# Optimization experiments

Measured on AMD Instinct MI355X. Metric: run time of the kernel, lower is better.

Reference implementation:

```python
import jax, jax.numpy as jnp
import numpy as np

B, T, V, E, D, F = 128, 64, 10000, 512, 512, 2048


def setup_inputs() -> dict:
    key = jax.random.key(0)
    ks = iter(jax.random.split(key, 40))
    def nrm(shape, s=0.02):
        return (jax.random.normal(next(ks), shape, jnp.float32) * s)
    inp = {
        "image_vectors": jax.random.normal(next(ks), (B, F), jnp.float32),
        "captions_ix": jax.random.randint(next(ks), (B, T), 0, V),
        "emb": nrm((V, E)),
        "W_init_h1": nrm((D, F)), "b_init_h1": jnp.zeros((D,), jnp.float32),
        "W_init_c1": nrm((D, F)), "b_init_c1": jnp.zeros((D,), jnp.float32),
        "W_init_h2": nrm((D, F)), "b_init_h2": jnp.zeros((D,), jnp.float32),
        "W_init_c2": nrm((D, F)), "b_init_c2": jnp.zeros((D,), jnp.float32),
        "W_ih1": nrm((4 * D, E)), "W_hh1": nrm((4 * D, D)), "b1": jnp.zeros((4 * D,), jnp.float32),
        "W_ih2": nrm((4 * D, 2 * D)), "W_hh2": nrm((4 * D, D)), "b2": jnp.zeros((4 * D,), jnp.float32),
        "Wv1": nrm((D, D)), "bv1": jnp.zeros((D,), jnp.float32),
        "Wo1": nrm((D, D)), "bo1": jnp.zeros((D,), jnp.float32),
        "Wv2": nrm((D, D)), "bv2": jnp.zeros((D,), jnp.float32),
        "Wo2": nrm((D, D)), "bo2": jnp.zeros((D,), jnp.float32),
        "W_logits": nrm((V, 3 * D)), "b_logits": jnp.zeros((V,), jnp.float32),
    }
    return inp


def _lstm(x, h0, c0, W_ih, W_hh, b):
    # x: [B,T,Din] -> hidden states [B,T,D]; PyTorch gate order (i,f,g,o), b = b_ih + b_hh.
    xp = jnp.einsum('btd,gd->btg', x, W_ih) + b  # precompute input projections
    def step(carry, xt):
        h, c = carry
        gates = xt + h @ W_hh.T
        i, f, g, o = jnp.split(gates, 4, axis=-1)
        c = jax.nn.sigmoid(f) * c + jax.nn.sigmoid(i) * jnp.tanh(g)
        h = jax.nn.sigmoid(o) * jnp.tanh(c)
        return (h, c), h
    _, hs = jax.lax.scan(step, (h0, c0), jnp.swapaxes(xp, 0, 1))
    return jnp.swapaxes(hs, 0, 1)


def reference(image_vectors, captions_ix, emb,
              W_init_h1, b_init_h1, W_init_c1, b_init_c1,
              W_init_h2, b_init_h2, W_init_c2, b_init_c2,
              W_ih1, W_hh1, b1, W_ih2, W_hh2, b2,
              Wv1, bv1, Wo1, bo1, Wv2, bv2, Wo2, bo2,
              W_logits, b_logits):
    h1 = image_vectors @ W_init_h1.T + b_init_h1
    c1 = image_vectors @ W_init_c1.T + b_init_c1
    h2 = image_vectors @ W_init_h2.T + b_init_h2
    c2 = image_vectors @ W_init_c2.T + b_init_c2
    x = emb[captions_ix]  # [B,T,E] (dropout p=0 -> identity)
    h1s = _lstm(x, h1, c1, W_ih1, W_hh1, b1)  # [B,T,D]; LSTM output == hidden state
    # MHA with key=value of length 1: softmax over one key is exactly 1, so the
    # output is out_proj(v_proj(key)) independent of the (growing prefix) query.
    attn1 = (h1s @ Wv1.T + bv1) @ Wo1.T + bo1  # [B,T,D]
    h2s = _lstm(jnp.concatenate([h1s, attn1], axis=-1), h2, c2, W_ih2, W_hh2, b2)
    attn2 = (h2s @ Wv2.T + bv2) @ Wo2.T + bo2
    out = jnp.concatenate([h2s, attn1, attn2], axis=-1)  # [B,T,3D]
    return out @ W_logits.T + b_logits  # [B,T,V]
```

## Files before the change

### kernel.cpp

```cpp
#include <hip/hip_runtime.h>
#include <stdint.h>

#define DEV __device__ __forceinline__

typedef short bf16x8 __attribute__((ext_vector_type(8)));
typedef float f32x4 __attribute__((ext_vector_type(4)));

DEV unsigned short f2bf(float f) {
  union { float f; uint32_t u; } v; v.f = f;
  return (unsigned short)((v.u + 0x7fffu + ((v.u >> 16) & 1u)) >> 16);
}
DEV float bf2f(unsigned short u) {
  union { uint32_t u; float f; } v; v.u = (uint32_t)u << 16; return v.f;
}

DEV float fsig(float x) { return 1.f / (1.f + __expf(-x)); }
DEV float ftanh(float x) { float e = __expf(2.f * x); return 1.f - 2.f / (e + 1.f); }

DEV void gload16(const void* g, void* lds) {
  __builtin_amdgcn_global_load_lds(
      (const __attribute__((address_space(1))) int*)(uintptr_t)g,
      (__attribute__((address_space(3))) int*)(uintptr_t)lds, 16, 0, 0);
}

template <int MODE>
__global__ __launch_bounds__(256) void gemm_nt(
    const unsigned short* __restrict__ A, int lda,
    const unsigned short* __restrict__ B, int ldb,
    void* __restrict__ P0, void* __restrict__ P1,
    void* __restrict__ P2, void* __restrict__ P3,
    int ldc, int ldc2,
    const float* __restrict__ bias,
    int K, int Nreal)
{
  __shared__ alignas(16) unsigned short Asm[128 * 32];
  __shared__ alignas(16) unsigned short Bsm[128 * 32];
  const int tid = threadIdx.x;
  const int wave = tid >> 6, lane = tid & 63;

  const int gx = gridDim.x;
  const int lin = blockIdx.y * gx + blockIdx.x;
  const int nwg = gx * gridDim.y;
  const int q = nwg >> 3, r = nwg & 7;
  const int xcd = lin & 7, i2 = lin >> 3;
  const int wg = (xcd < r ? xcd * (q + 1) : r * (q + 1) + (xcd - r) * q) + i2;
  const int m0 = (wg % gx) * 128, n0 = (wg / gx) * 128;

  const int wr = wave >> 1, wc = wave & 1;
  f32x4 acc[4][4] = {};

  const int q0 = tid, q1 = tid + 256;
  const unsigned short* Ag0 = A + (size_t)(m0 + (q0 >> 2)) * lda + (q0 & 3) * 8;
  const unsigned short* Ag1 = A + (size_t)(m0 + (q1 >> 2)) * lda + (q1 & 3) * 8;
  const unsigned short* Bg0 = B + (size_t)(n0 + (q0 >> 2)) * ldb + (q0 & 3) * 8;
  const unsigned short* Bg1 = B + (size_t)(n0 + (q1 >> 2)) * ldb + (q1 & 3) * 8;
  char* As0 = (char*)Asm + wave * 1024;  char* As1 = As0 + 4096;
  char* Bs0 = (char*)Bsm + wave * 1024;  char* Bs1 = Bs0 + 4096;

  const int ra = wr * 64 + (lane & 15);
  const int rb = wc * 64 + (lane & 15);
  const int kb = (lane >> 4) * 16;

  for (int k0 = 0; k0 < K; k0 += 32) {
    gload16(Ag0 + k0, As0);
    gload16(Ag1 + k0, As1);
    gload16(Bg0 + k0, Bs0);
    gload16(Bg1 + k0, Bs1);
    __syncthreads();
    bf16x8 af[4], bfr[4];
#pragma unroll
    for (int i = 0; i < 4; ++i)
      af[i] = *(const bf16x8*)((const char*)Asm + (ra + i * 16) * 64 + kb);
#pragma unroll
    for (int i = 0; i < 4; ++i)
      bfr[i] = *(const bf16x8*)((const char*)Bsm + (rb + i * 16) * 64 + kb);
#pragma unroll
    for (int mi = 0; mi < 4; ++mi)
#pragma unroll
      for (int ni = 0; ni < 4; ++ni)
        acc[mi][ni] = __builtin_amdgcn_mfma_f32_16x16x32_bf16(af[mi], bfr[ni], acc[mi][ni], 0, 0, 0);
    __syncthreads();
  }

  const int row0 = m0 + wr * 64 + (lane >> 4) * 4;
  const int col0 = n0 + wc * 64 + (lane & 15);

  if constexpr (MODE == 2) {
#pragma unroll
    for (int mi = 0; mi < 4; ++mi) {
      const int rowb = row0 + mi * 16;
      const int dd = rowb >> 2;
      const float4 b4 = *(const float4*)&bias[rowb];
#pragma unroll
      for (int ni = 0; ni < 4; ++ni) {
        const int col = col0 + ni * 16;
        const int tt = col & 63, bb = col >> 6;
        float4 v;
        v.x = acc[mi][ni][0] + b4.x;
        v.y = acc[mi][ni][1] + b4.y;
        v.z = acc[mi][ni][2] + b4.z;
        v.w = acc[mi][ni][3] + b4.w;
        const int wgid = (bb >> 4) * 16 + (dd >> 5);
        const int ww = (dd >> 3) & 3, mi2 = (dd >> 2) & 1, ln = (dd & 3) * 16 + (bb & 15);
        ((float4*)P0)[((((size_t)tt * 128 + wgid) * 4 + ww) * 2 + mi2) * 64 + ln] = v;
      }
    }
    return;
  }

#pragma unroll
  for (int mi = 0; mi < 4; ++mi) {
#pragma unroll
    for (int ni = 0; ni < 4; ++ni) {
      const int col = col0 + ni * 16;
      if (col >= Nreal) continue;
      const float bs = bias ? bias[col] : 0.f;
#pragma unroll
      for (int rr = 0; rr < 4; ++rr) {
        const int row = row0 + mi * 16 + rr;
        const float v = acc[mi][ni][rr] + bs;
        if constexpr (MODE == 1) {
          ((unsigned short*)P0)[(size_t)row * ldc + col] = f2bf(v);
          if (P1) ((unsigned short*)P1)[(size_t)row * ldc2 + col] = f2bf(v);
        } else if constexpr (MODE == 4) {
          const unsigned short ad = ((const unsigned short*)P1)[(size_t)row * ldc2 + col];
          ((unsigned short*)P0)[(size_t)row * ldc + col] = f2bf(v + bf2f(ad));
        } else {
          const int seg = col >> 9, cc = col & 511;
          if (seg == 0)      ((unsigned short*)P0)[(size_t)row * 512 + cc] = f2bf(v);
          else if (seg == 1) ((float*)P1)[(size_t)row * 512 + cc] = v;
          else if (seg == 2) ((unsigned short*)P2)[(size_t)row * 512 + cc] = f2bf(v);
          else               ((float*)P3)[(size_t)row * 512 + cc] = v;
        }
      }
    }
  }
}

__global__ __launch_bounds__(512, 2) void gemm256(
    const unsigned short* __restrict__ A, int lda,
    const unsigned short* __restrict__ B, int ldb,
    float* __restrict__ C, int ldc,
    const float* __restrict__ bias, int K, int Nreal)
{
  __shared__ alignas(16) unsigned short Lds[2][2][16384];
  const int tid = threadIdx.x;
  const int wave = tid >> 6, lane = tid & 63;
  const int fr = lane & 15, kq = lane >> 4;

  const int gx = gridDim.x;
  const int lin = blockIdx.y * gx + blockIdx.x;
  const int nwg = gx * gridDim.y;
  const int q8 = nwg >> 3, r8 = nwg & 7;
  const int xcd = lin & 7, i2 = lin >> 3;
  const int wg = (xcd < r8 ? xcd * (q8 + 1) : r8 * (q8 + 1) + (xcd - r8) * q8) + i2;
  const int m0 = (wg % gx) * 256, n0 = (wg / gx) * 256;

  const int wr = wave >> 2, wc = wave & 3;

  const unsigned short* srcA[4];
  const unsigned short* srcB[4];
  int dstO[4];
#pragma unroll
  for (int s = 0; s < 4; ++s) {
    const int c = tid + s * 512;
    const int row = c >> 3, qp = (c & 7) ^ (row & 7);
    srcA[s] = A + (size_t)(m0 + row) * lda + qp * 8;
    srcB[s] = B + (size_t)(n0 + row) * ldb + qp * 8;
    dstO[s] = (wave * 64 + s * 512) * 16;
  }

  const int NT = K >> 6;
#define STAGE256(kt, buf)                                            \
  {                                                                  \
    _Pragma("unroll")                                                \
    for (int s = 0; s < 4; ++s)                                      \
      gload16(srcA[s] + (kt) * 64, (char*)&Lds[buf][0][0] + dstO[s]);\
    _Pragma("unroll")                                                \
    for (int s = 0; s < 4; ++s)                                      \
      gload16(srcB[s] + (kt) * 64, (char*)&Lds[buf][1][0] + dstO[s]);\
  }
  STAGE256(0, 0);
  STAGE256(1, 1);

  f32x4 acc[8][4] = {};
  const int slot0 = (kq ^ (fr & 7)) * 16;

  for (int kt = 0; kt < NT; ++kt) {
    asm volatile("s_waitcnt vmcnt(8)" ::: "memory");
    __builtin_amdgcn_sched_barrier(0);
    __builtin_amdgcn_s_barrier();
    __builtin_amdgcn_sched_barrier(0);
    const char* bufA = (const char*)&Lds[kt & 1][0][0];
    const char* bufB = (const char*)&Lds[kt & 1][1][0];
    bf16x8 Bf[4][2];
#pragma unroll
    for (int n = 0; n < 4; ++n) {
      const char* bb = bufB + (wc * 64 + n * 16 + fr) * 128;
      Bf[n][0] = *(const bf16x8*)(bb + slot0);
      Bf[n][1] = *(const bf16x8*)(bb + (slot0 ^ 64));
    }
#pragma unroll
    for (int q = 0; q < 4; ++q) {
      bf16x8 Af[2][2];
#pragma unroll
      for (int m2 = 0; m2 < 2; ++m2) {
        const char* ab = bufA + (wr * 128 + q * 32 + m2 * 16 + fr) * 128;
        Af[m2][0] = *(const bf16x8*)(ab + slot0);
        Af[m2][1] = *(const bf16x8*)(ab + (slot0 ^ 64));
      }
      __builtin_amdgcn_s_setprio(1);
#pragma unroll
      for (int m2 = 0; m2 < 2; ++m2)
#pragma unroll
        for (int n = 0; n < 4; ++n) {
          acc[q * 2 + m2][n] = __builtin_amdgcn_mfma_f32_16x16x32_bf16(
              Af[m2][0], Bf[n][0], acc[q * 2 + m2][n], 0, 0, 0);
          acc[q * 2 + m2][n] = __builtin_amdgcn_mfma_f32_16x16x32_bf16(
              Af[m2][1], Bf[n][1], acc[q * 2 + m2][n], 0, 0, 0);
        }
      __builtin_amdgcn_s_setprio(0);
    }
    __builtin_amdgcn_sched_barrier(0);
    __builtin_amdgcn_s_barrier();
    __builtin_amdgcn_sched_barrier(0);
    const int kn = (kt + 2 < NT) ? kt + 2 : 0;
    STAGE256(kn, kt & 1);
  }

#pragma unroll
  for (int mf = 0; mf < 8; ++mf) {
    const int row = m0 + wr * 128 + mf * 16 + kq * 4;
#pragma unroll
    for (int n = 0; n < 4; ++n) {
      const int col = n0 + wc * 64 + n * 16 + fr;
      if (col < Nreal) {
        const float bs = bias[col];
#pragma unroll
        for (int rr = 0; rr < 4; ++rr)
          __builtin_nontemporal_store(acc[mf][n][rr] + bs,
                                      &C[(size_t)(row + rr) * ldc + col]);
      }
    }
  }
#undef STAGE256
}

__global__ __launch_bounds__(256, 1) void lstm_fused(
    const unsigned short* __restrict__ Whh1, const unsigned short* __restrict__ Whh2,
    const unsigned short* __restrict__ Weff2r,
    const unsigned short* __restrict__ h01, const unsigned short* __restrict__ h02,
    const float* __restrict__ c1st, const float* __restrict__ c2st,
    const float* __restrict__ xpr,
    const float* __restrict__ beff2,
    unsigned short* __restrict__ hx1, unsigned short* __restrict__ hx2,
    unsigned short* __restrict__ hcat,
    int* __restrict__ flags)
{
  __shared__ unsigned short Wsm[8][128][64];
  __shared__ uint32_t Hst[16][16];
  const int tid = threadIdx.x;
  const bool role2 = blockIdx.x >= 128;
  const int wg = role2 ? blockIdx.x - 128 : blockIdx.x;
  const int g = wg >> 4, s = wg & 15;
  const int w = tid >> 6, lane = tid & 63, fr = lane & 15, kq = lane >> 4;

  {
    const unsigned short* Whh = role2 ? Whh2 : Whh1;
    const int m = tid >> 1;
    const int row = (m & 3) * 512 + s * 32 + (m >> 2);
    const unsigned short* src = Whh + (size_t)row * 512 + (tid & 1) * 256;
#pragma unroll 4
    for (int cc = 0; cc < 32; ++cc) {
      const int k = (tid & 1) * 256 + cc * 8;
      uint4 v = *(const uint4*)(src + cc * 8);
      const int kblk = k >> 6, c = (k & 63) >> 3, sl = c ^ (m & 7);
      *(uint4*)((char*)&Wsm[kblk][m][0] + sl * 16) = v;
    }
  }

  const int b = g * 16 + fr;
  const int d0 = s * 32 + w * 8 + kq;
  const float* c0 = role2 ? c2st : c1st;
  float c_r[2];
  c_r[0] = c0[b * 512 + d0];
  c_r[1] = c0[b * 512 + d0 + 4];
  __syncthreads();

  int* fl1 = flags + g * 16;
  int* fl2 = flags + 128 + g * 16;
  int* flown = role2 ? fl2 : fl1;
  unsigned short* hxown = role2 ? hx2 : hx1;
  const unsigned short* hinit = role2 ? h02 : h01;
  const int colbase = (role2 ? 0 : 512) + s * 32;
  const float4* xv = (const float4*)xpr + ((size_t)(wg * 4 + w) * 2) * 64 + lane;
  float4 be0 = {0, 0, 0, 0}, be1 = {0, 0, 0, 0};
  if (role2) {
    be0 = *(const float4*)(beff2 + s * 128 + w * 32 + kq * 4);
    be1 = *(const float4*)(beff2 + s * 128 + w * 32 + 16 + kq * 4);
  }
  const size_t hxg = (size_t)g * 8192;

  for (int t = 0; t < 64; ++t) {
    f32x4 acc[2] = {};
    float4 xg0, xg1;

    if (!role2) {
      xg0 = xv[(size_t)t * 65536];
      xg1 = xv[(size_t)t * 65536 + 64];
      if (t) {
        if (w == 1) {
          for (;;) {
            bool ok = true;
            if (lane < 16)
              ok = __hip_atomic_load(fl1 + lane, __ATOMIC_RELAXED,
                                     __HIP_MEMORY_SCOPE_AGENT) >= t;
            if (__all(ok)) break;
            __builtin_amdgcn_s_sleep(1);
          }
        }
        __syncthreads();
      }
      bf16x8 hf[16];
      if (t == 0) {
#pragma unroll
        for (int kk = 0; kk < 16; ++kk)
          hf[kk] = *(const bf16x8*)(hinit + (size_t)b * 512 + kk * 32 + kq * 8);
      } else {
        const unsigned short* hb = hx1 + (size_t)(t - 1) * 65536 + hxg + fr * 32 + kq * 8;
#pragma unroll
        for (int kk = 0; kk < 16; ++kk)
          hf[kk] = *(const bf16x8*)(hb + kk * 512);
      }
#pragma unroll
      for (int kk = 0; kk < 16; ++kk) {
        const int kblk = kk >> 1, cbase = (kk & 1) * 4 + kq;
#pragma unroll
        for (int mi = 0; mi < 2; ++mi) {
          const int m = w * 32 + mi * 16 + fr;
          const int sl = cbase ^ (m & 7);
          const bf16x8 af = *(const bf16x8*)((const char*)&Wsm[kblk][m][0] + sl * 16);
          acc[mi] = __builtin_amdgcn_mfma_f32_16x16x32_bf16(af, hf[kk], acc[mi], 0, 0, 0);
        }
      }
    } else {
      xg0 = be0; xg1 = be1;
      if (w == 1) {
        for (;;) {
          bool ok = true;
          if (lane < 16)
            ok = __hip_atomic_load(fl1 + lane, __ATOMIC_RELAXED,
                                   __HIP_MEMORY_SCOPE_AGENT) >= t + 1;
          if (__all(ok)) break;
          __builtin_amdgcn_s_sleep(1);
        }
      }
      __syncthreads();
      const unsigned short* h1b = hx1 + (size_t)t * 65536 + hxg + fr * 32 + kq * 8;
      bf16x8 hf1[16];
#pragma unroll
      for (int kk = 0; kk < 16; ++kk)
        hf1[kk] = *(const bf16x8*)(h1b + kk * 512);
      const bf16x8* wr = (const bf16x8*)Weff2r + (size_t)s * 32 * 256 + tid;
#pragma unroll
      for (int kk = 0; kk < 8; ++kk) {
#pragma unroll
        for (int mi = 0; mi < 2; ++mi)
          acc[mi] = __builtin_amdgcn_mfma_f32_16x16x32_bf16(
              wr[(kk * 2 + mi) * 256], hf1[kk], acc[mi], 0, 0, 0);
      }
      if (t) {
        if (w == 1) {
          for (;;) {
            bool ok = true;
            if (lane < 16)
              ok = __hip_atomic_load(fl2 + lane, __ATOMIC_RELAXED,
                                     __HIP_MEMORY_SCOPE_AGENT) >= t;
            if (__all(ok)) break;
            __builtin_amdgcn_s_sleep(1);
          }
        }
        __syncthreads();
      }
      bf16x8 hf2[16];
      if (t == 0) {
#pragma unroll
        for (int kk = 0; kk < 16; ++kk)
          hf2[kk] = *(const bf16x8*)(hinit + (size_t)b * 512 + kk * 32 + kq * 8);
      } else {
        const unsigned short* hb = hx2 + (size_t)(t - 1) * 65536 + hxg + fr * 32 + kq * 8;
#pragma unroll
        for (int kk = 0; kk < 16; ++kk)
          hf2[kk] = *(const bf16x8*)(hb + kk * 512);
      }
#pragma unroll
      for (int kk = 8; kk < 16; ++kk) {
#pragma unroll
        for (int mi = 0; mi < 2; ++mi)
          acc[mi] = __builtin_amdgcn_mfma_f32_16x16x32_bf16(
              wr[(kk * 2 + mi) * 256], hf1[kk], acc[mi], 0, 0, 0);
      }
#pragma unroll
      for (int kk = 0; kk < 16; ++kk) {
        const int kblk = kk >> 1, cbase = (kk & 1) * 4 + kq;
#pragma unroll
        for (int mi = 0; mi < 2; ++mi) {
          const int m = w * 32 + mi * 16 + fr;
          const int sl = cbase ^ (m & 7);
          const bf16x8 af = *(const bf16x8*)((const char*)&Wsm[kblk][m][0] + sl * 16);
          acc[mi] = __builtin_amdgcn_mfma_f32_16x16x32_bf16(af, hf2[kk], acc[mi], 0, 0, 0);
        }
      }
    }

    unsigned short hn[2];
#pragma unroll
    for (int mi = 0; mi < 2; ++mi) {
      const float4 xg = mi ? xg1 : xg0;
      const float iv = acc[mi][0] + xg.x;
      const float fv = acc[mi][1] + xg.y;
      const float gv = acc[mi][2] + xg.z;
      const float ov = acc[mi][3] + xg.w;
      const float c = fsig(fv) * c_r[mi] + fsig(iv) * ftanh(gv);
      c_r[mi] = c;
      hn[mi] = f2bf(fsig(ov) * ftanh(c));
    }

    const uint32_t pk = (uint32_t)hn[0] | ((uint32_t)hn[1] << 16);
    const uint32_t y = (uint32_t)__shfl_xor((int)pk, 16);
    const uint32_t word = (kq & 1) ? __builtin_amdgcn_perm(pk, y, 0x07060302)
                                   : __builtin_amdgcn_perm(y, pk, 0x05040100);
    Hst[fr][w * 4 + ((kq & 1) ? 2 + (kq >> 1) : (kq >> 1))] = word;
    __syncthreads();

    if (w == 0) {
      const uint4 v = *(const uint4*)&Hst[lane >> 2][(lane & 3) * 4];
      unsigned short* dst = hxown + (size_t)t * 65536 + hxg + s * 512 + lane * 8;
      __hip_atomic_store((unsigned long long*)dst, ((const unsigned long long*)&v)[0],
                         __ATOMIC_RELAXED, __HIP_MEMORY_SCOPE_AGENT);
      __hip_atomic_store((unsigned long long*)(dst + 4), ((const unsigned long long*)&v)[1],
                         __ATOMIC_RELAXED, __HIP_MEMORY_SCOPE_AGENT);
      asm volatile("s_waitcnt vmcnt(0)" ::: "memory");
      if (lane == 0)
        __hip_atomic_store(flown + s, t + 1, __ATOMIC_RELAXED, __HIP_MEMORY_SCOPE_AGENT);
      const int row = (g * 16 + (lane >> 2)) * 64 + t;
      *(uint4*)(hcat + (size_t)row * 1024 + colbase + (lane & 3) * 8) = v;
    }
  }
}

struct CastJobs {
  const float* src[12];
  unsigned short* dst[12];
  long nreal4[12];
  long cum4[13];
  int n;
};

__global__ void cast_multi4(CastJobs J) {
  const long total = J.cum4[J.n];
  for (long i = (long)blockIdx.x * blockDim.x + threadIdx.x; i < total;
       i += (long)gridDim.x * blockDim.x) {
    int s = 0;
    while (i >= J.cum4[s + 1]) ++s;
    const long off = i - J.cum4[s];
    float4 v = {0.f, 0.f, 0.f, 0.f};
    if (off < J.nreal4[s]) v = ((const float4*)J.src[s])[off];
    ushort4 o;
    o.x = f2bf(v.x); o.y = f2bf(v.y); o.z = f2bf(v.z); o.w = f2bf(v.w);
    ((ushort4*)J.dst[s])[off] = o;
  }
}

__global__ void prep1(const float* __restrict__ Wv1, const float* __restrict__ Wv2,
                      const float* __restrict__ Wihl1, const float* __restrict__ Wihl2,
                      const float* __restrict__ b1, const float* __restrict__ b2,
                      const float* __restrict__ bih1, const float* __restrict__ bic1,
                      const float* __restrict__ bih2, const float* __restrict__ bic2,
                      const float* __restrict__ Wo1, const float* __restrict__ bv1,
                      const float* __restrict__ bo1,
                      const float* __restrict__ Wo2, const float* __restrict__ bv2,
                      const float* __restrict__ bo2,
                      unsigned short* __restrict__ WvT1, unsigned short* __restrict__ WvT2,
                      unsigned short* __restrict__ Wp1, unsigned short* __restrict__ Wp2,
                      float* __restrict__ bp1, float* __restrict__ bp2,
                      float* __restrict__ bcat,
                      float* __restrict__ bc1, float* __restrict__ bc2)
{
  const long NTOT = 924672;
  for (long id = (long)blockIdx.x * blockDim.x + threadIdx.x; id < NTOT;
       id += (long)gridDim.x * blockDim.x) {
    if (id < 131072) {
      const int m = (int)(id >> 6), kb = (int)(id & 63) * 8;
      const float* sp = Wihl1 + (size_t)((m & 3) * 512 + (m >> 2)) * 512 + kb;
      unsigned short o[8];
#pragma unroll
      for (int e = 0; e < 8; ++e) o[e] = f2bf(sp[e]);
      *(uint4*)(Wp1 + (size_t)m * 512 + kb) = *(const uint4*)o;
    } else if (id < 393216) {
      const long j = id - 131072;
      const int m = (int)(j >> 7), kb = (int)(j & 127) * 8;
      const float* sp = Wihl2 + (size_t)((m & 3) * 512 + (m >> 2)) * 1024 + kb;
      unsigned short o[8];
#pragma unroll
      for (int e = 0; e < 8; ++e) o[e] = f2bf(sp[e]);
      *(uint4*)(Wp2 + (size_t)m * 1024 + kb) = *(const uint4*)o;
    } else if (id < 917504) {
      const long t = id - 393216;
      const int which = (int)(t >> 18);
      const int u = (int)(t & 262143), a = u >> 9, bb = u & 511;
      (which ? WvT2 : WvT1)[u] = f2bf((which ? Wv2 : Wv1)[(size_t)bb * 512 + a]);
    } else if (id < 921600) {
      const int t = (int)(id - 917504);
      if (t < 2048) bp1[t] = b1[(t & 3) * 512 + (t >> 2)];
      else { const int m = t - 2048; bp2[m] = b2[(m & 3) * 512 + (m >> 2)]; }
    } else if (id < 923648) {
      const int i = (int)(id - 921600);
      const float* sarr[4] = {bih1, bic1, bih2, bic2};
      bcat[i] = sarr[i >> 9][i & 511];
    } else {
      const int i = (int)(id - 923648);
      const float* Wo = (i >= 512) ? Wo2 : Wo1;
      const float* bv = (i >= 512) ? bv2 : bv1;
      const float* bo = (i >= 512) ? bo2 : bo1;
      float* bc = (i >= 512) ? bc2 : bc1;
      const int r = i & 511;
      float sacc = bo[r];
      for (int k = 0; k < 512; k += 4) {
        const float4 wv = *(const float4*)(Wo + (size_t)r * 512 + k);
        const float4 bb = *(const float4*)(bv + k);
        sacc += wv.x * bb.x + wv.y * bb.y + wv.z * bb.z + wv.w * bb.w;
      }
      bc[r] = sacc;
    }
  }
}

__global__ void gather_rows(const int* __restrict__ ix, const float* __restrict__ emb,
                            unsigned short* __restrict__ x) {
  const int row = blockIdx.x;
  const int e = ix[row];
  const float4* s = (const float4*)(emb + (size_t)e * 512) + threadIdx.x * 2;
  const float4 a = s[0], b = s[1];
  unsigned short o[8] = {f2bf(a.x), f2bf(a.y), f2bf(a.z), f2bf(a.w),
                         f2bf(b.x), f2bf(b.y), f2bf(b.z), f2bf(b.w)};
  *(uint4*)(x + (size_t)row * 512 + threadIdx.x * 8) = *(const uint4*)o;
}

__global__ void reorder_wbf(const unsigned short* __restrict__ W,
                            unsigned short* __restrict__ R) {
  const int id = blockIdx.x * blockDim.x + threadIdx.x;
  const int tid = id & 255, mi = (id >> 8) & 1, kk = (id >> 9) & 15, s = id >> 13;
  const int w = tid >> 6, lane = tid & 63, fr = lane & 15, kq = lane >> 4;
  const int row = s * 128 + w * 32 + mi * 16 + fr;
  const int col = kk * 32 + kq * 8;
  *((uint4*)R + id) = *(const uint4*)(W + (size_t)row * 512 + col);
}

__global__ void bias2(const unsigned short* __restrict__ Wl, const float* __restrict__ blog,
                      const unsigned short* __restrict__ Wp2, const float* __restrict__ bp2,
                      const float* __restrict__ bc1, const float* __restrict__ bc2,
                      float* __restrict__ blcat, float* __restrict__ beff2) {
  const int lane = threadIdx.x & 63;
  if (blockIdx.x < 512) {
    const int m = blockIdx.x * 4 + (threadIdx.x >> 6);
    const unsigned short* row = Wp2 + (size_t)m * 1024 + 512;
    float sum = 0.f;
    for (int k = lane; k < 512; k += 64) sum += bf2f(row[k]) * bc1[k];
#pragma unroll
    for (int mm = 32; mm; mm >>= 1) sum += __shfl_xor(sum, mm, 64);
    if (lane == 0) beff2[m] = bp2[m] + sum;
  } else {
    const int j = (blockIdx.x - 512) * 4 + (threadIdx.x >> 6);
    const unsigned short* row = Wl + (size_t)j * 1536;
    float sum = 0.f;
    for (int k = lane; k < 512; k += 64) {
      sum += bf2f(row[512 + k]) * bc1[k];
      sum += bf2f(row[1024 + k]) * bc2[k];
    }
#pragma unroll
    for (int mm = 32; mm; mm >>= 1) sum += __shfl_xor(sum, mm, 64);
    if (lane == 0) blcat[j] = blog[j] + sum;
  }
}

extern "C" void kernel_launch(void* const* d_in, const int* in_sizes, int n_in,
                              void* d_out, int out_size, void* d_ws, size_t ws_size,
                              hipStream_t stream) {
  (void)in_sizes; (void)n_in; (void)out_size; (void)ws_size;
  const float* img    = (const float*)d_in[0];
  const int*   ix     = (const int*)d_in[1];
  const float* emb    = (const float*)d_in[2];
  const float* Wih1f  = (const float*)d_in[3];
  const float* bih1   = (const float*)d_in[4];
  const float* Wic1f  = (const float*)d_in[5];
  const float* bic1   = (const float*)d_in[6];
  const float* Wih2f  = (const float*)d_in[7];
  const float* bih2   = (const float*)d_in[8];
  const float* Wic2f  = (const float*)d_in[9];
  const float* bic2   = (const float*)d_in[10];
  const float* Wihl1  = (const float*)d_in[11];
  const float* Whhl1  = (const float*)d_in[12];
  const float* b1     = (const float*)d_in[13];
  const float* Wihl2  = (const float*)d_in[14];
  const float* Whhl2  = (const float*)d_in[15];
  const float* b2     = (const float*)d_in[16];
  const float* Wv1    = (const float*)d_in[17];
  const float* bv1    = (const float*)d_in[18];
  const float* Wo1    = (const float*)d_in[19];
  const float* bo1    = (const float*)d_in[20];
  const float* Wv2    = (const float*)d_in[21];
  const float* bv2    = (const float*)d_in[22];
  const float* Wo2    = (const float*)d_in[23];
  const float* bo2    = (const float*)d_in[24];
  const float* Wlog   = (const float*)d_in[25];
  const float* blog   = (const float*)d_in[26];
  float* out = (float*)d_out;

  char* p = (char*)d_ws;
  auto al = [&](size_t bytes) { char* r = p; p += (bytes + 255) & ~(size_t)255; return r; };
  unsigned short* Wp1    = (unsigned short*)al((size_t)2048 * 512 * 2);
  unsigned short* Whh1_b = (unsigned short*)al((size_t)2048 * 512 * 2);
  unsigned short* Wp2    = (unsigned short*)al((size_t)2048 * 1024 * 2);
  unsigned short* Whh2_b = (unsigned short*)al((size_t)2048 * 512 * 2);
  unsigned short* WvT1   = (unsigned short*)al((size_t)512 * 512 * 2);
  unsigned short* Wo1_b  = (unsigned short*)al((size_t)512 * 512 * 2);
  unsigned short* WvT2   = (unsigned short*)al((size_t)512 * 512 * 2);
  unsigned short* Wo2_b  = (unsigned short*)al((size_t)512 * 512 * 2);
  unsigned short* Wc1T   = (unsigned short*)al((size_t)512 * 512 * 2);
  unsigned short* Wc2T   = (unsigned short*)al((size_t)512 * 512 * 2);
  unsigned short* Wlog_b = (unsigned short*)al((size_t)10240 * 1536 * 2);
  unsigned short* Wcat   = (unsigned short*)al((size_t)10240 * 1024 * 2);
  unsigned short* Weff2  = (unsigned short*)al((size_t)2048 * 512 * 2);
  unsigned short* Weff2r = (unsigned short*)al((size_t)2048 * 512 * 2);
  unsigned short* Wh1i_b = (unsigned short*)al((size_t)512 * 2048 * 2);
  unsigned short* Wc1i_b = (unsigned short*)al((size_t)512 * 2048 * 2);
  unsigned short* Wh2i_b = (unsigned short*)al((size_t)512 * 2048 * 2);
  unsigned short* Wc2i_b = (unsigned short*)al((size_t)512 * 2048 * 2);
  unsigned short* img_b  = (unsigned short*)al((size_t)128 * 2048 * 2);
  unsigned short* x_b    = (unsigned short*)al((size_t)8192 * 512 * 2);
  float*          xpr    = (float*)al((size_t)8192 * 2048 * 4);
  unsigned short* hcat   = (unsigned short*)al((size_t)8192 * 1024 * 2);
  unsigned short* hx1    = (unsigned short*)al((size_t)64 * 128 * 512 * 2);
  unsigned short* hx2    = (unsigned short*)al((size_t)64 * 128 * 512 * 2);
  unsigned short* h01    = (unsigned short*)al((size_t)128 * 512 * 2);
  unsigned short* h02    = (unsigned short*)al((size_t)128 * 512 * 2);
  float*          c1st   = (float*)al((size_t)128 * 512 * 4);
  float*          c2st   = (float*)al((size_t)128 * 512 * 4);
  float*          bcat   = (float*)al((size_t)2048 * 4);
  float*          bp1    = (float*)al((size_t)2048 * 4);
  float*          bp2    = (float*)al((size_t)2048 * 4);
  float*          bc1    = (float*)al((size_t)512 * 4);
  float*          bc2    = (float*)al((size_t)512 * 4);
  float*          beff2  = (float*)al((size_t)2048 * 4);
  float*          blcat  = (float*)al((size_t)10240 * 4);
  int*            flags  = (int*)al(2048);

  hipMemsetAsync(flags, 0, 2048, stream);

  CastJobs J = {};
  auto addjob = [&](const float* s, unsigned short* d, long nreal, long ntot) {
    J.src[J.n] = s; J.dst[J.n] = d; J.nreal4[J.n] = nreal / 4;
    J.cum4[J.n + 1] = J.cum4[J.n] + ntot / 4; ++J.n;
  };
  addjob(img,   img_b,  (long)128 * 2048,   (long)128 * 2048);
  addjob(Whhl1, Whh1_b, (long)2048 * 512,   (long)2048 * 512);
  addjob(Whhl2, Whh2_b, (long)2048 * 512,   (long)2048 * 512);
  addjob(Wo1,   Wo1_b,  (long)512 * 512,    (long)512 * 512);
  addjob(Wo2,   Wo2_b,  (long)512 * 512,    (long)512 * 512);
  addjob(Wih1f, Wh1i_b, (long)512 * 2048,   (long)512 * 2048);
  addjob(Wic1f, Wc1i_b, (long)512 * 2048,   (long)512 * 2048);
  addjob(Wih2f, Wh2i_b, (long)512 * 2048,   (long)512 * 2048);
  addjob(Wic2f, Wc2i_b, (long)512 * 2048,   (long)512 * 2048);
  addjob(Wlog,  Wlog_b, (long)10000 * 1536, (long)10240 * 1536);
  cast_multi4<<<2048, 256, 0, stream>>>(J);

  prep1<<<1024, 256, 0, stream>>>(Wv1, Wv2, Wihl1, Wihl2, b1, b2,
                                  bih1, bic1, bih2, bic2,
                                  Wo1, bv1, bo1, Wo2, bv2, bo2,
                                  WvT1, WvT2, Wp1, Wp2, bp1, bp2, bcat, bc1, bc2);

  gather_rows<<<8192, 64, 0, stream>>>(ix, emb, x_b);

  gemm_nt<1><<<dim3(4, 4), 256, 0, stream>>>(
      WvT1, 512, Wo1_b, 512, Wc1T, nullptr, nullptr, nullptr, 512, 0, nullptr, 512, 512);
  gemm_nt<1><<<dim3(4, 4), 256, 0, stream>>>(
      WvT2, 512, Wo2_b, 512, Wc2T, nullptr, nullptr, nullptr, 512, 0, nullptr, 512, 512);

  gemm_nt<4><<<dim3(16, 4), 256, 0, stream>>>(
      Wp2 + 512, 1024, Wc1T, 512, Weff2, Wp2, nullptr, nullptr, 512, 1024, nullptr, 512, 512);
  reorder_wbf<<<512, 256, 0, stream>>>(Weff2, Weff2r);
  bias2<<<3012, 256, 0, stream>>>(Wlog_b, blog, Wp2, bp2, bc1, bc2, blcat, beff2);

  gemm_nt<4><<<dim3(80, 4), 256, 0, stream>>>(
      Wlog_b + 1024, 1536, Wc2T, 512, Wcat, Wlog_b, nullptr, nullptr, 1024, 1536,
      nullptr, 512, 512);
  gemm_nt<1><<<dim3(80, 4), 256, 0, stream>>>(
      Wlog_b + 512, 1536, Wc1T, 512, Wcat + 512, nullptr, nullptr, nullptr, 1024, 0,
      nullptr, 512, 512);

  gemm_nt<3><<<dim3(1, 16), 256, 0, stream>>>(
      img_b, 2048, Wh1i_b, 2048, h01, c1st, h02, c2st, 0, 0, bcat, 2048, 2048);

  gemm_nt<2><<<dim3(16, 64), 256, 0, stream>>>(
      Wp1, 512, x_b, 512, xpr, nullptr, nullptr, nullptr, 0, 0, bp1, 512, 8192);

  lstm_fused<<<256, 256, 0, stream>>>(
      Whh1_b, Whh2_b, Weff2r, h01, h02, c1st, c2st, xpr, beff2, hx1, hx2, hcat, flags);

  gemm256<<<dim3(32, 40), 512, 0, stream>>>(
      hcat, 1024, Wcat, 1024, out, 10000, blcat, 1024, 10000);
}
```

Measured before the change: 842.6 us.

## Batch independent prep GEMMs into grouped launches and merge small prep kernels

Replaces the templated per-mode gemm_nt launches with a gemm_batch kernel that takes a table of up to four GEMM jobs, each selected by block index. The seven small weight-prep GEMMs run as two launches, and reorder_wbf and bias2 merge into one combo kernel. This removes launch gaps and lets small grids share the GPU. It drops the XCD-aware block remapping and turns the epilogue mode into a runtime branch, which may cost some cache locality and instruction efficiency.

```diff
diff --git a/kernel.cpp b/kernel.cpp
--- a/kernel.cpp
+++ b/kernel.cpp
@@ -23,37 +23,34 @@
       (__attribute__((address_space(3))) int*)(uintptr_t)lds, 16, 0, 0);
 }
 
-template <int MODE>
-__global__ __launch_bounds__(256) void gemm_nt(
-    const unsigned short* __restrict__ A, int lda,
-    const unsigned short* __restrict__ B, int ldb,
-    void* __restrict__ P0, void* __restrict__ P1,
-    void* __restrict__ P2, void* __restrict__ P3,
-    int ldc, int ldc2,
-    const float* __restrict__ bias,
-    int K, int Nreal)
-{
+struct GJob {
+  const unsigned short* A; const unsigned short* B;
+  void *P0, *P1, *P2, *P3;
+  const float* bias;
+  int lda, ldb, ldc, ldc2, K, Nreal, gx, mode, wg_end, pad;
+};
+struct GJobs { GJob j[4]; };
+
+__global__ __launch_bounds__(256) void gemm_batch(GJobs JB) {
+  int ji = 0;
+  while ((int)blockIdx.x >= JB.j[ji].wg_end) ++ji;
+  const GJob J = JB.j[ji];
+  const int wg = blockIdx.x - (ji ? JB.j[ji - 1].wg_end : 0);
+
   __shared__ alignas(16) unsigned short Asm[128 * 32];
   __shared__ alignas(16) unsigned short Bsm[128 * 32];
   const int tid = threadIdx.x;
   const int wave = tid >> 6, lane = tid & 63;
-
-  const int gx = gridDim.x;
-  const int lin = blockIdx.y * gx + blockIdx.x;
-  const int nwg = gx * gridDim.y;
-  const int q = nwg >> 3, r = nwg & 7;
-  const int xcd = lin & 7, i2 = lin >> 3;
-  const int wg = (xcd < r ? xcd * (q + 1) : r * (q + 1) + (xcd - r) * q) + i2;
-  const int m0 = (wg % gx) * 128, n0 = (wg / gx) * 128;
-
+  const int m0 = (wg % J.gx) * 128, n0 = (wg / J.gx) * 128;
   const int wr = wave >> 1, wc = wave & 1;
+
   f32x4 acc[4][4] = {};
 
   const int q0 = tid, q1 = tid + 256;
-  const unsigned short* Ag0 = A + (size_t)(m0 + (q0 >> 2)) * lda + (q0 & 3) * 8;
-  const unsigned short* Ag1 = A + (size_t)(m0 + (q1 >> 2)) * lda + (q1 & 3) * 8;
-  const unsigned short* Bg0 = B + (size_t)(n0 + (q0 >> 2)) * ldb + (q0 & 3) * 8;
-  const unsigned short* Bg1 = B + (size_t)(n0 + (q1 >> 2)) * ldb + (q1 & 3) * 8;
+  const unsigned short* Ag0 = J.A + (size_t)(m0 + (q0 >> 2)) * J.lda + (q0 & 3) * 8;
+  const unsigned short* Ag1 = J.A + (size_t)(m0 + (q1 >> 2)) * J.lda + (q1 & 3) * 8;
+  const unsigned short* Bg0 = J.B + (size_t)(n0 + (q0 >> 2)) * J.ldb + (q0 & 3) * 8;
+  const unsigned short* Bg1 = J.B + (size_t)(n0 + (q1 >> 2)) * J.ldb + (q1 & 3) * 8;
   char* As0 = (char*)Asm + wave * 1024;  char* As1 = As0 + 4096;
   char* Bs0 = (char*)Bsm + wave * 1024;  char* Bs1 = Bs0 + 4096;
 
@@ -61,7 +58,7 @@
   const int rb = wc * 64 + (lane & 15);
   const int kb = (lane >> 4) * 16;
 
-  for (int k0 = 0; k0 < K; k0 += 32) {
+  for (int k0 = 0; k0 < J.K; k0 += 32) {
     gload16(Ag0 + k0, As0);
     gload16(Ag1 + k0, As1);
     gload16(Bg0 + k0, Bs0);
@@ -85,12 +82,12 @@
   const int row0 = m0 + wr * 64 + (lane >> 4) * 4;
   const int col0 = n0 + wc * 64 + (lane & 15);
 
-  if constexpr (MODE == 2) {
+  if (J.mode == 2) {
 #pragma unroll
     for (int mi = 0; mi < 4; ++mi) {
       const int rowb = row0 + mi * 16;
       const int dd = rowb >> 2;
-      const float4 b4 = *(const float4*)&bias[rowb];
+      const float4 b4 = *(const float4*)&J.bias[rowb];
 #pragma unroll
       for (int ni = 0; ni < 4; ++ni) {
         const int col = col0 + ni * 16;
@@ -102,7 +99,7 @@
         v.w = acc[mi][ni][3] + b4.w;
         const int wgid = (bb >> 4) * 16 + (dd >> 5);
         const int ww = (dd >> 3) & 3, mi2 = (dd >> 2) & 1, ln = (dd & 3) * 16 + (bb & 15);
-        ((float4*)P0)[((((size_t)tt * 128 + wgid) * 4 + ww) * 2 + mi2) * 64 + ln] = v;
+        ((float4*)J.P0)[((((size_t)tt * 128 + wgid) * 4 + ww) * 2 + mi2) * 64 + ln] = v;
       }
     }
     return;
@@ -113,24 +110,24 @@
 #pragma unroll
     for (int ni = 0; ni < 4; ++ni) {
       const int col = col0 + ni * 16;
-      if (col >= Nreal) continue;
-      const float bs = bias ? bias[col] : 0.f;
+      if (col >= J.Nreal) continue;
+      const float bs = J.bias ? J.bias[col] : 0.f;
 #pragma unroll
       for (int rr = 0; rr < 4; ++rr) {
         const int row = row0 + mi * 16 + rr;
         const float v = acc[mi][ni][rr] + bs;
-        if constexpr (MODE == 1) {
-          ((unsigned short*)P0)[(size_t)row * ldc + col] = f2bf(v);
-          if (P1) ((unsigned short*)P1)[(size_t)row * ldc2 + col] = f2bf(v);
-        } else if constexpr (MODE == 4) {
-          const unsigned short ad = ((const unsigned short*)P1)[(size_t)row * ldc2 + col];
-          ((unsigned short*)P0)[(size_t)row * ldc + col] = f2bf(v + bf2f(ad));
+        if (J.mode == 1) {
+          ((unsigned short*)J.P0)[(size_t)row * J.ldc + col] = f2bf(v);
+          if (J.P1) ((unsigned short*)J.P1)[(size_t)row * J.ldc2 + col] = f2bf(v);
+        } else if (J.mode == 4) {
+          const unsigned short ad = ((const unsigned short*)J.P1)[(size_t)row * J.ldc2 + col];
+          ((unsigned short*)J.P0)[(size_t)row * J.ldc + col] = f2bf(v + bf2f(ad));
         } else {
           const int seg = col >> 9, cc = col & 511;
-          if (seg == 0)      ((unsigned short*)P0)[(size_t)row * 512 + cc] = f2bf(v);
-          else if (seg == 1) ((float*)P1)[(size_t)row * 512 + cc] = v;
-          else if (seg == 2) ((unsigned short*)P2)[(size_t)row * 512 + cc] = f2bf(v);
-          else               ((float*)P3)[(size_t)row * 512 + cc] = v;
+          if (seg == 0)      ((unsigned short*)J.P0)[(size_t)row * 512 + cc] = f2bf(v);
+          else if (seg == 1) ((float*)J.P1)[(size_t)row * 512 + cc] = v;
+          else if (seg == 2) ((unsigned short*)J.P2)[(size_t)row * 512 + cc] = f2bf(v);
+          else               ((float*)J.P3)[(size_t)row * 512 + cc] = v;
         }
       }
     }
@@ -547,23 +544,21 @@
   *(uint4*)(x + (size_t)row * 512 + threadIdx.x * 8) = *(const uint4*)o;
 }
 
-__global__ void reorder_wbf(const unsigned short* __restrict__ W,
-                            unsigned short* __restrict__ R) {
-  const int id = blockIdx.x * blockDim.x + threadIdx.x;
-  const int tid = id & 255, mi = (id >> 8) & 1, kk = (id >> 9) & 15, s = id >> 13;
-  const int w = tid >> 6, lane = tid & 63, fr = lane & 15, kq = lane >> 4;
-  const int row = s * 128 + w * 32 + mi * 16 + fr;
-  const int col = kk * 32 + kq * 8;
-  *((uint4*)R + id) = *(const uint4*)(W + (size_t)row * 512 + col);
-}
-
-__global__ void bias2(const unsigned short* __restrict__ Wl, const float* __restrict__ blog,
+__global__ void combo(const unsigned short* __restrict__ W, unsigned short* __restrict__ R,
+                      const unsigned short* __restrict__ Wl, const float* __restrict__ blog,
                       const unsigned short* __restrict__ Wp2, const float* __restrict__ bp2,
                       const float* __restrict__ bc1, const float* __restrict__ bc2,
                       float* __restrict__ blcat, float* __restrict__ beff2) {
   const int lane = threadIdx.x & 63;
   if (blockIdx.x < 512) {
-    const int m = blockIdx.x * 4 + (threadIdx.x >> 6);
+    const int id = blockIdx.x * 256 + threadIdx.x;
+    const int tid = id & 255, mi = (id >> 8) & 1, kk = (id >> 9) & 15, s = id >> 13;
+    const int w = tid >> 6, ln = tid & 63, fr = ln & 15, kq = ln >> 4;
+    const int row = s * 128 + w * 32 + mi * 16 + fr;
+    const int col = kk * 32 + kq * 8;
+    *((uint4*)R + id) = *(const uint4*)(W + (size_t)row * 512 + col);
+  } else if (blockIdx.x < 1024) {
+    const int m = (blockIdx.x - 512) * 4 + (threadIdx.x >> 6);
     const unsigned short* row = Wp2 + (size_t)m * 1024 + 512;
     float sum = 0.f;
     for (int k = lane; k < 512; k += 64) sum += bf2f(row[k]) * bc1[k];
@@ -571,7 +566,7 @@
     for (int mm = 32; mm; mm >>= 1) sum += __shfl_xor(sum, mm, 64);
     if (lane == 0) beff2[m] = bp2[m] + sum;
   } else {
-    const int j = (blockIdx.x - 512) * 4 + (threadIdx.x >> 6);
+    const int j = (blockIdx.x - 1024) * 4 + (threadIdx.x >> 6);
     const unsigned short* row = Wl + (size_t)j * 1536;
     float sum = 0.f;
     for (int k = lane; k < 512; k += 64) {
@@ -682,28 +677,32 @@
 
   gather_rows<<<8192, 64, 0, stream>>>(ix, emb, x_b);
 
-  gemm_nt<1><<<dim3(4, 4), 256, 0, stream>>>(
-      WvT1, 512, Wo1_b, 512, Wc1T, nullptr, nullptr, nullptr, 512, 0, nullptr, 512, 512);
-  gemm_nt<1><<<dim3(4, 4), 256, 0, stream>>>(
-      WvT2, 512, Wo2_b, 512, Wc2T, nullptr, nullptr, nullptr, 512, 0, nullptr, 512, 512);
-
-  gemm_nt<4><<<dim3(16, 4), 256, 0, stream>>>(
-      Wp2 + 512, 1024, Wc1T, 512, Weff2, Wp2, nullptr, nullptr, 512, 1024, nullptr, 512, 512);
-  reorder_wbf<<<512, 256, 0, stream>>>(Weff2, Weff2r);
-  bias2<<<3012, 256, 0, stream>>>(Wlog_b, blog, Wp2, bp2, bc1, bc2, blcat, beff2);
-
-  gemm_nt<4><<<dim3(80, 4), 256, 0, stream>>>(
-      Wlog_b + 1024, 1536, Wc2T, 512, Wcat, Wlog_b, nullptr, nullptr, 1024, 1536,
-      nullptr, 512, 512);
-  gemm_nt<1><<<dim3(80, 4), 256, 0, stream>>>(
-      Wlog_b + 512, 1536, Wc1T, 512, Wcat + 512, nullptr, nullptr, nullptr, 1024, 0,
-      nullptr, 512, 512);
-
-  gemm_nt<3><<<dim3(1, 16), 256, 0, stream>>>(
-      img_b, 2048, Wh1i_b, 2048, h01, c1st, h02, c2st, 0, 0, bcat, 2048, 2048);
-
-  gemm_nt<2><<<dim3(16, 64), 256, 0, stream>>>(
-      Wp1, 512, x_b, 512, xpr, nullptr, nullptr, nullptr, 0, 0, bp1, 512, 8192);
+  {
+    GJobs B = {};
+    B.j[0] = {Wp1, x_b, xpr, nullptr, nullptr, nullptr, bp1,
+              512, 512, 0, 0, 512, 8192, 16, 2, 1024, 0};
+    B.j[1] = {WvT1, Wo1_b, Wc1T, nullptr, nullptr, nullptr, nullptr,
+              512, 512, 512, 0, 512, 512, 4, 1, 1040, 0};
+    B.j[2] = {WvT2, Wo2_b, Wc2T, nullptr, nullptr, nullptr, nullptr,
+              512, 512, 512, 0, 512, 512, 4, 1, 1056, 0};
+    B.j[3] = {img_b, Wh1i_b, h01, c1st, h02, c2st, bcat,
+              2048, 2048, 0, 0, 2048, 2048, 1, 3, 1072, 0};
+    gemm_batch<<<1072, 256, 0, stream>>>(B);
+  }
+
+  {
+    GJobs B = {};
+    B.j[0] = {Wlog_b + 1024, Wc2T, Wcat, Wlog_b, nullptr, nullptr, nullptr,
+              1536, 512, 1024, 1536, 512, 512, 80, 4, 320, 0};
+    B.j[1] = {Wlog_b + 512, Wc1T, Wcat + 512, nullptr, nullptr, nullptr, nullptr,
+              1536, 512, 1024, 0, 512, 512, 80, 1, 640, 0};
+    B.j[2] = {Wp2 + 512, Wc1T, Weff2, Wp2, nullptr, nullptr, nullptr,
+              1024, 512, 512, 1024, 512, 512, 16, 4, 704, 0};
+    gemm_batch<<<704, 256, 0, stream>>>(B);
+  }
+
+  combo<<<3524, 256, 0, stream>>>(Weff2, Weff2r, Wlog_b, blog, Wp2, bp2,
+                                  bc1, bc2, blcat, beff2);
 
   lstm_fused<<<256, 256, 0, stream>>>(
       Whh1_b, Whh2_b, Weff2r, h01, h02, c1st, c2st, xpr, beff2, hx1, hx2, hcat, flags);
```

New measurement: 763.7 us (median of 2 runs). 9.4% less time.
